# Optimization experiments

Measured on AMD Instinct MI355X. Metric: run time of the kernel, lower is better.

The kernel has to match this reference:

```python
import jax, jax.numpy as jnp
import numpy as np

WINDOW = 7
NUM_HEADS = 16
HEAD_DIM = 32  # dim 512 / 16 heads
SCALE = HEAD_DIM ** -0.5


def _relative_position_index(ws: int) -> np.ndarray:
    coords = np.stack(np.meshgrid(np.arange(ws), np.arange(ws), indexing='ij'))  # [2, ws, ws]
    flat = coords.reshape(2, -1)  # [2, N]
    rel = flat[:, :, None] - flat[:, None, :]  # [2, N, N]
    rel = rel.transpose(1, 2, 0)  # [N, N, 2]
    rh = (rel[:, :, 0] + ws - 1) * (2 * ws - 1)
    rw = rel[:, :, 1] + ws - 1
    return (rh + rw).astype(np.int32)  # [N, N]

REL_IDX = jnp.asarray(_relative_position_index(WINDOW))  # [49, 49]


def setup_inputs() -> dict:
    key = jax.random.key(0)
    ks = jax.random.split(key, 4)
    B, N, C = 4096, WINDOW * WINDOW, 512
    x = jax.random.normal(ks[0], (B, N, C), dtype=jnp.float32)
    qkv_w = jax.random.normal(ks[1], (C, 3 * C), dtype=jnp.float32) * (C ** -0.5)
    qkv_b = jnp.zeros((3 * C,), dtype=jnp.float32)
    proj_w = jax.random.normal(ks[2], (C, C), dtype=jnp.float32) * (C ** -0.5)
    proj_b = jnp.zeros((C,), dtype=jnp.float32)
    bias_table = jax.random.normal(ks[3], ((2 * WINDOW - 1) ** 2, NUM_HEADS), dtype=jnp.float32) * 0.02
    return {"x": x, "qkv_w": qkv_w, "qkv_b": qkv_b, "proj_w": proj_w,
            "proj_b": proj_b, "bias_table": bias_table}


def reference(x, qkv_w, qkv_b, proj_w, proj_b, bias_table):
    B, N, C = x.shape
    # QKV projection -> [B, N, 3, H, D] -> q/k/v [B, H, N, D]
    qkv = (x @ qkv_w + qkv_b).reshape(B, N, 3, NUM_HEADS, HEAD_DIM)
    qkv = jnp.transpose(qkv, (2, 0, 3, 1, 4))
    q, k, v = qkv[0], qkv[1], qkv[2]
    attn = jnp.einsum('bhnd,bhmd->bhnm', q * SCALE, k)  # [B, H, N, N]
    # relative position bias gather: [N*N, H] -> [1, H, N, N]
    bias = bias_table[REL_IDX.reshape(-1)].reshape(N, N, NUM_HEADS)
    attn = attn + jnp.transpose(bias, (2, 0, 1))[None]
    attn = jax.nn.softmax(attn, axis=-1)
    out = jnp.einsum('bhnm,bhmd->bhnd', attn, v)  # [B, H, N, D]
    out = jnp.transpose(out, (0, 2, 1, 3)).reshape(B, N, C)
    return out @ proj_w + proj_b
```

## Files before the change

kernel.cpp:

```cpp
#include <hip/hip_runtime.h>

typedef _Float16 h16;
typedef __attribute__((ext_vector_type(4))) _Float16 h16x4;
typedef __attribute__((ext_vector_type(8))) _Float16 h16x8;
typedef __attribute__((ext_vector_type(4))) float f32x4;

#define QSCALE 0.25505653882616254f
#define LOG2E  1.4426950408889634f
#define MFMA16(a, b, c) __builtin_amdgcn_mfma_f32_16x16x16f16(a, b, c, 0, 0, 0)
#define MFMA32(a, b, c) __builtin_amdgcn_mfma_f32_16x16x32_f16(a, b, c, 0, 0, 0)

#define O_BYTES 205520896ULL
#define W1F_OFF (O_BYTES)
#define W2T_OFF (W1F_OFF + 1572864ULL)
#define BF_OFF  (W2T_OFF + 524288ULL)

__global__ __launch_bounds__(256) void wa_prep(
    const float* __restrict__ qkv_w, const float* __restrict__ proj_w,
    const float* __restrict__ table,
    h16* __restrict__ w1F, h16* __restrict__ w2T, float* __restrict__ biasF) {
  __shared__ h16 T[32][33];
  const int b = blockIdx.x, tid = threadIdx.x;
  if (b < 256) {
    int tx = tid & 31, ty = tid >> 5;
    int bo = b & 15, bc = b >> 4;
    #pragma unroll
    for (int i = 0; i < 4; ++i) {
      int c = bc * 32 + ty + 8 * i, o = bo * 32 + tx;
      T[ty + 8 * i][tx] = (h16)proj_w[c * 512 + o];
    }
    __syncthreads();
    #pragma unroll
    for (int i = 0; i < 4; ++i) {
      int o_l = ty + 8 * i;
      w2T[(size_t)(bo * 32 + o_l) * 512 + bc * 32 + tx] = T[tx][o_l];
    }
  } else if (b < 640) {
    int chunk = (b - 256) * 256 + tid;
    int lane = chunk & 63;
    int rest = chunk >> 6;
    int f  = rest % 12;
    int kt = (rest / 12) & 7;
    int wv = (rest / 96) & 3;
    int g  = rest / 384;
    int s = f >> 2, d = (f >> 1) & 1, ks = f & 1;
    int l15 = lane & 15, lg = lane >> 4;
    int o = s * 512 + g * 128 + wv * 32 + d * 16 + l15;
    int k0 = kt * 64 + ks * 32 + lg * 8;
    float sc = (s == 0) ? QSCALE : 1.0f;
    h16x8 v;
    #pragma unroll
    for (int e = 0; e < 8; ++e)
      v[e] = (h16)(qkv_w[(size_t)(k0 + e) * 1536 + o] * sc);
    *(h16x8*)(w1F + (size_t)chunk * 8) = v;
  } else {
    int t = (b - 640) * 256 + tid;
    int lane = t & 63, jt = (t >> 6) & 3, qt = (t >> 8) & 3, head = t >> 10;
    int l15 = lane & 15, lg = lane >> 4;
    int q = qt * 16 + l15;
    float4 v;
    #pragma unroll
    for (int r = 0; r < 4; ++r) {
      int j = jt * 16 + lg * 4 + r;
      float val = -1e30f;
      if (j < 49 && q < 49) {
        int rel = (q / 7 - j / 7 + 6) * 13 + (q % 7 - j % 7 + 6);
        val = table[rel * 16 + head] * LOG2E;
      }
      ((float*)&v)[r] = val;
    }
    ((float4*)biasF)[t] = v;
  }
}

__global__ __launch_bounds__(256, 3) void wa_qkv_attn(
    const float* __restrict__ x, const float* __restrict__ qkv_b,
    const h16* __restrict__ w1F, const float* __restrict__ biasF,
    h16* __restrict__ O) {
  __shared__ __align__(16) char lds[50176];
  const int tid = threadIdx.x;
  const int wave = tid >> 6, lane = tid & 63;
  const int l15 = lane & 15, lg = lane >> 4;
  const int sw = l15 & 7;
  const int lbid = (blockIdx.x & 7) * 1024 + (blockIdx.x >> 3);
  const int w = lbid >> 1, gp = lbid & 1;
  const size_t rowbase = (size_t)w * 49;

  #pragma unroll
  for (int p = 0; p < 13; ++p) {
    int idx = tid + p * 256;
    if (idx < 3136) {
      int r = idx >> 6, c = idx & 63;
      const float* src = x + (rowbase + r) * 512 + c * 8;
      float4 a = *(const float4*)(src);
      float4 bb = *(const float4*)(src + 4);
      h16x8 h = { (h16)a.x, (h16)a.y, (h16)a.z, (h16)a.w,
                  (h16)bb.x, (h16)bb.y, (h16)bb.z, (h16)bb.w };
      *(h16x8*)(lds + r * 1024 + ((c ^ (r & 7)) << 4)) = h;
    }
  }
  __syncthreads();

  int xbA[4], xbB[4];
  #pragma unroll
  for (int t = 0; t < 4; ++t) {
    int row = (t < 3) ? (16 * t + l15) : 48;
    int swt = (t < 3) ? sw : 0;
    xbA[t] = row * 1024 + ((lg ^ swt) << 4);
    xbB[t] = row * 1024 + (((4 + lg) ^ swt) << 4);
  }
  const h16x4 ones = (h16x4){(h16)1.f, (h16)1.f, (h16)1.f, (h16)1.f};
  const float4* bF4 = (const float4*)biasF;

#define WLOAD8(DST, KT) {                                                  \
    _Pragma("unroll") for (int f8 = 0; f8 < 8; ++f8)                       \
      DST[f8] = *(const h16x8*)(wb + (size_t)(KT) * 6144 + f8 * 512); }

#define WLOAD4V(DST, KT) {                                                 \
    _Pragma("unroll") for (int f4 = 0; f4 < 4; ++f4)                       \
      DST[f4] = *(const h16x8*)(wb + (size_t)(KT) * 6144 + (8 + f4) * 512); }

#define STEP_QK(KT, W) {                                                   \
    h16x8 xf[4];                                                           \
    _Pragma("unroll") for (int t = 0; t < 4; ++t)                          \
      xf[t] = *(const h16x8*)(lds + xbA[t] + (KT) * 128);                  \
    __builtin_amdgcn_s_setprio(1);                                         \
    _Pragma("unroll") for (int d = 0; d < 2; ++d)                          \
    _Pragma("unroll") for (int t = 0; t < 4; ++t) {                        \
      accQ[d][t] = MFMA32(W[d*2],     xf[t], accQ[d][t]);                  \
      accK[d][t] = MFMA32(W[4 + d*2], xf[t], accK[d][t]);                  \
    }                                                                      \
    __builtin_amdgcn_s_setprio(0);                                         \
    _Pragma("unroll") for (int t = 0; t < 4; ++t)                          \
      xf[t] = *(const h16x8*)(lds + xbB[t] + (KT) * 128);                  \
    __builtin_amdgcn_s_setprio(1);                                         \
    _Pragma("unroll") for (int d = 0; d < 2; ++d)                          \
    _Pragma("unroll") for (int t = 0; t < 4; ++t) {                        \
      accQ[d][t] = MFMA32(W[d*2 + 1],     xf[t], accQ[d][t]);              \
      accK[d][t] = MFMA32(W[4 + d*2 + 1], xf[t], accK[d][t]);              \
    }                                                                      \
    __builtin_amdgcn_s_setprio(0); }

#define STEP_V(KT, W) {                                                    \
    h16x8 xf[4];                                                           \
    _Pragma("unroll") for (int t = 0; t < 4; ++t)                          \
      xf[t] = *(const h16x8*)(lds + xbA[t] + (KT) * 128);                  \
    __builtin_amdgcn_s_setprio(1);                                         \
    _Pragma("unroll") for (int d = 0; d < 2; ++d)                          \
    _Pragma("unroll") for (int t = 0; t < 4; ++t)                          \
      accV[t][d] = MFMA32(xf[t], W[d*2], accV[t][d]);                      \
    __builtin_amdgcn_s_setprio(0);                                         \
    _Pragma("unroll") for (int t = 0; t < 4; ++t)                          \
      xf[t] = *(const h16x8*)(lds + xbB[t] + (KT) * 128);                  \
    __builtin_amdgcn_s_setprio(1);                                         \
    _Pragma("unroll") for (int d = 0; d < 2; ++d)                          \
    _Pragma("unroll") for (int t = 0; t < 4; ++t)                          \
      accV[t][d] = MFMA32(xf[t], W[d*2 + 1], accV[t][d]);                  \
    __builtin_amdgcn_s_setprio(0); }

#define PROCESS_HEAD(G) {                                                  \
    const int head = (G) * 4 + wave;                                       \
    const h16* wb = w1F + ((size_t)((G) * 4 + wave) * 8) * 6144 + lane * 8;\
    h16x4 Qh[2][4], Kh[2][4], Vh[4][2];                                    \
     {                          \
      f32x4 accQ[2][4], accK[2][4];                                        \
      _Pragma("unroll") for (int d = 0; d < 2; ++d)                        \
      _Pragma("unroll") for (int t = 0; t < 4; ++t) {                      \
        accQ[d][t] = (f32x4){0.f, 0.f, 0.f, 0.f};                          \
        accK[d][t] = (f32x4){0.f, 0.f, 0.f, 0.f};                          \
      }                                                                    \
      h16x8 WA[8], WB[8];                                                  \
      WLOAD8(WA, 0);                                                       \
      for (int kt2 = 0; kt2 < 4; ++kt2) {                                  \
        WLOAD8(WB, 2 * kt2 + 1);                                           \
        STEP_QK(2 * kt2, WA);                                              \
        if (kt2 < 3) WLOAD8(WA, 2 * kt2 + 2);                              \
        STEP_QK(2 * kt2 + 1, WB);                                          \
      }                                                                    \
      _Pragma("unroll") for (int d = 0; d < 2; ++d) {                      \
        float bq[4], bk[4];                                                \
        _Pragma("unroll") for (int r = 0; r < 4; ++r) {                    \
          bq[r] = qkv_b[head * 32 + 16 * d + 4 * lg + r] * QSCALE;         \
          bk[r] = qkv_b[512 + head * 32 + 16 * d + 4 * lg + r];            \
        }                                                                  \
        _Pragma("unroll") for (int t = 0; t < 4; ++t)                      \
        _Pragma("unroll") for (int r = 0; r < 4; ++r) {                    \
          Qh[d][t][r] = (h16)(accQ[d][t][r] + bq[r]);                      \
          Kh[d][t][r] = (h16)(accK[d][t][r] + bk[r]);                      \
        }                                                                  \
      }                                                                    \
    }                                                                      \
     {                  \
      f32x4 accV[4][2];                                                    \
      _Pragma("unroll") for (int t = 0; t < 4; ++t)                        \
      _Pragma("unroll") for (int d = 0; d < 2; ++d)                        \
        accV[t][d] = (f32x4){0.f, 0.f, 0.f, 0.f};                          \
      h16x8 VA[4], VB[4];                                                  \
      WLOAD4V(VA, 0);                                                      \
      for (int kt2 = 0; kt2 < 4; ++kt2) {                                  \
        WLOAD4V(VB, 2 * kt2 + 1);                                          \
        STEP_V(2 * kt2, VA);                                               \
        if (kt2 < 3) WLOAD4V(VA, 2 * kt2 + 2);                             \
        STEP_V(2 * kt2 + 1, VB);                                           \
      }                                                                    \
      _Pragma("unroll") for (int d = 0; d < 2; ++d) {                      \
        float bv = qkv_b[1024 + head * 32 + 16 * d + l15];                 \
        _Pragma("unroll") for (int t = 0; t < 4; ++t)                      \
        _Pragma("unroll") for (int r = 0; r < 4; ++r)                      \
          Vh[t][d][r] = (h16)(accV[t][d][r] + bv);                         \
      }                                                                    \
    }                                                                      \
                             \
    f32x4 st[4][4];                                                        \
    __builtin_amdgcn_s_setprio(1);                                         \
    _Pragma("unroll") for (int jt = 0; jt < 4; ++jt)                       \
    _Pragma("unroll") for (int qt = 0; qt < 4; ++qt) {                     \
      float4 bvv = bF4[(head * 16 + qt * 4 + jt) * 64 + lane];             \
      f32x4 c0 = { bvv.x, bvv.y, bvv.z, bvv.w };                           \
      st[jt][qt] = MFMA16(Kh[0][jt], Qh[0][qt], c0);                       \
      st[jt][qt] = MFMA16(Kh[1][jt], Qh[1][qt], st[jt][qt]);               \
    }                                                                      \
    __builtin_amdgcn_s_setprio(0);                                         \
    h16x4 pf[4][4];                                                        \
    _Pragma("unroll") for (int qt = 0; qt < 4; ++qt)                       \
    _Pragma("unroll") for (int jt = 0; jt < 4; ++jt) {                     \
      h16x4 p;                                                             \
      _Pragma("unroll") for (int r = 0; r < 4; ++r)                        \
        p[r] = (h16)exp2f(st[jt][qt][r]);                                  \
      pf[jt][qt] = p;                                                      \
    }                                                                      \
    f32x4 ss[4];                                                           \
    _Pragma("unroll") for (int qt = 0; qt < 4; ++qt)                       \
      ss[qt] = (f32x4){0.f, 0.f, 0.f, 0.f};                                \
    f32x4 ot[2][4];                                                        \
    _Pragma("unroll") for (int d = 0; d < 2; ++d)                          \
    _Pragma("unroll") for (int qt = 0; qt < 4; ++qt)                       \
      ot[d][qt] = (f32x4){0.f, 0.f, 0.f, 0.f};                             \
    __builtin_amdgcn_s_setprio(1);                                         \
    _Pragma("unroll") for (int jt = 0; jt < 4; ++jt)                       \
    _Pragma("unroll") for (int qt = 0; qt < 4; ++qt) {                     \
      ss[qt] = MFMA16(ones, pf[jt][qt], ss[qt]);                           \
      _Pragma("unroll") for (int d = 0; d < 2; ++d)                        \
        ot[d][qt] = MFMA16(Vh[jt][d], pf[jt][qt], ot[d][qt]);              \
    }                                                                      \
    __builtin_amdgcn_s_setprio(0);                                         \
    _Pragma("unroll") for (int qt = 0; qt < 4; ++qt) {                     \
      int q = 16 * qt + l15;                                               \
      float ri = 1.0f / ss[qt][0];                                         \
      if (q < 49) {                                                        \
        h16* gdst = O + (rowbase + q) * 512 + head * 32 + 4 * lg;          \
        _Pragma("unroll") for (int d = 0; d < 2; ++d) {                    \
          h16x4 ov;                                                        \
          _Pragma("unroll") for (int r = 0; r < 4; ++r)                    \
            ov[r] = (h16)(ot[d][qt][r] * ri);                              \
          *(h16x4*)(gdst + 16 * d) = ov;                                   \
        }                                                                  \
      }                                                                    \
    } }

  PROCESS_HEAD(gp * 2);
  PROCESS_HEAD(gp * 2 + 1);
#undef PROCESS_HEAD
#undef STEP_QK
#undef STEP_V
#undef WLOAD8
#undef WLOAD4V
}

__global__ __launch_bounds__(256, 3) void wa_proj(
    const h16* __restrict__ O, const h16* __restrict__ w2T,
    const float* __restrict__ proj_b, float* __restrict__ out) {
  __shared__ __align__(16) char lds[32768];
  char* Ac = lds;
  char* Bc = lds + 16384;
  const int tid = threadIdx.x;
  const int wave = tid >> 6, lane = tid & 63;
  const int l15 = lane & 15, lg = lane >> 4;
  const int lbid = (blockIdx.x & 7) * 784 + (blockIdx.x >> 3);
  const int rowt = lbid >> 2, colt = lbid & 3;
  const int wr = wave >> 1, wc = wave & 1;

  f32x4 acc[4][4];
  #pragma unroll
  for (int a = 0; a < 4; ++a)
    #pragma unroll
    for (int b = 0; b < 4; ++b) acc[a][b] = (f32x4){0.f, 0.f, 0.f, 0.f};

  h16x8 pre[8];
  #pragma unroll
  for (int p = 0; p < 8; ++p) {
    int idx = tid + p * 256;
    int r = (idx >> 3) & 127, c = idx & 7;
    pre[p] = (idx < 1024)
        ? *(const h16x8*)(O   + (size_t)(rowt * 128 + r) * 512 + c * 8)
        : *(const h16x8*)(w2T + (size_t)(colt * 128 + r) * 512 + c * 8);
  }
  #pragma unroll
  for (int p = 0; p < 8; ++p) {
    int idx = tid + p * 256;
    int r = (idx >> 3) & 127, c = idx & 7;
    char* dst = ((idx < 1024) ? Ac : Bc) + r * 128 + ((c ^ (r & 7)) << 4);
    *(h16x8*)dst = pre[p];
  }
  __syncthreads();

  for (int kt = 0; kt < 8; ++kt) {
    if (kt < 7) {
      #pragma unroll
      for (int p = 0; p < 8; ++p) {
        int idx = tid + p * 256;
        int r = (idx >> 3) & 127, c = idx & 7;
        pre[p] = (idx < 1024)
            ? *(const h16x8*)(O   + (size_t)(rowt * 128 + r) * 512 + (kt + 1) * 64 + c * 8)
            : *(const h16x8*)(w2T + (size_t)(colt * 128 + r) * 512 + (kt + 1) * 64 + c * 8);
      }
    }
    #pragma unroll
    for (int kh = 0; kh < 2; ++kh) {
      const int cc = kh * 4 + lg;
      const int sw = (l15 & 7);
      h16x8 af[4], bf[4];
      #pragma unroll
      for (int mt = 0; mt < 4; ++mt) {
        int r = wr * 64 + 16 * mt + l15;
        af[mt] = *(const h16x8*)(Ac + r * 128 + ((cc ^ sw) << 4));
      }
      #pragma unroll
      for (int nt = 0; nt < 4; ++nt) {
        int r = wc * 64 + 16 * nt + l15;
        bf[nt] = *(const h16x8*)(Bc + r * 128 + ((cc ^ sw) << 4));
      }
      __builtin_amdgcn_s_setprio(1);
      #pragma unroll
      for (int mt = 0; mt < 4; ++mt)
        #pragma unroll
        for (int nt = 0; nt < 4; ++nt)
          acc[mt][nt] = MFMA32(af[mt], bf[nt], acc[mt][nt]);
      __builtin_amdgcn_s_setprio(0);
    }
    __syncthreads();
    if (kt < 7) {
      #pragma unroll
      for (int p = 0; p < 8; ++p) {
        int idx = tid + p * 256;
        int r = (idx >> 3) & 127, c = idx & 7;
        char* dst = ((idx < 1024) ? Ac : Bc) + r * 128 + ((c ^ (r & 7)) << 4);
        *(h16x8*)dst = pre[p];
      }
      __syncthreads();
    }
  }
  #pragma unroll
  for (int nt = 0; nt < 4; ++nt) {
    int col = colt * 128 + wc * 64 + nt * 16 + l15;
    float pb = proj_b[col];
    #pragma unroll
    for (int mt = 0; mt < 4; ++mt) {
      int row = rowt * 128 + wr * 64 + mt * 16 + 4 * lg;
      #pragma unroll
      for (int r = 0; r < 4; ++r)
        out[(size_t)(row + r) * 512 + col] = acc[mt][nt][r] + pb;
    }
  }
}

extern "C" void kernel_launch(void* const* d_in, const int* in_sizes, int n_in,
                              void* d_out, int out_size, void* d_ws, size_t ws_size,
                              hipStream_t stream) {
  const float* x          = (const float*)d_in[0];
  const float* qkv_w      = (const float*)d_in[1];
  const float* qkv_b      = (const float*)d_in[2];
  const float* proj_w     = (const float*)d_in[3];
  const float* proj_b     = (const float*)d_in[4];
  const float* bias_table = (const float*)d_in[5];
  float* out = (float*)d_out;

  char* ws = (char*)d_ws;
  h16*   O     = (h16*)ws;
  h16*   w1F   = (h16*)(ws + W1F_OFF);
  h16*   w2T   = (h16*)(ws + W2T_OFF);
  float* biasF = (float*)(ws + BF_OFF);

  wa_prep<<<704, 256, 0, stream>>>(qkv_w, proj_w, bias_table, w1F, w2T, biasF);
  wa_qkv_attn<<<8192, 256, 0, stream>>>(x, qkv_b, w1F, biasF, O);
  wa_proj<<<1568 * 4, 256, 0, stream>>>(O, w2T, proj_b, out);
}
```

Baseline: 701.1 us.

## Pre-swizzle proj weights into MFMA fragment layout and drop double-buffered QKV loads

The prep kernel now writes proj_w directly in MFMA B-fragment order, so the projection kernel reads B operands straight from global memory (L2) instead of staging them through LDS. This halves the projection kernel's LDS footprint and its staging traffic, at the cost of uncoalesced-per-iteration global fragment loads that are not prefetched. Separately, the QKV/attention kernel replaces its software double-buffered weight loads with a simple non-unrolled loop that loads and consumes one k-tile at a time. That lowers register pressure but exposes the weight-load latency.

After: 699.3 us. About the same (-0.3%).

```diff
diff --git a/kernel.cpp b/kernel.cpp
--- a/kernel.cpp
+++ b/kernel.cpp
@@ -12,31 +12,30 @@
 
 #define O_BYTES 205520896ULL
 #define W1F_OFF (O_BYTES)
-#define W2T_OFF (W1F_OFF + 1572864ULL)
-#define BF_OFF  (W2T_OFF + 524288ULL)
+#define W2F_OFF (W1F_OFF + 1572864ULL)
+#define BF_OFF  (W2F_OFF + 524288ULL)
 
 __global__ __launch_bounds__(256) void wa_prep(
     const float* __restrict__ qkv_w, const float* __restrict__ proj_w,
     const float* __restrict__ table,
-    h16* __restrict__ w1F, h16* __restrict__ w2T, float* __restrict__ biasF) {
-  __shared__ h16 T[32][33];
+    h16* __restrict__ w1F, h16* __restrict__ w2F, float* __restrict__ biasF) {
   const int b = blockIdx.x, tid = threadIdx.x;
-  if (b < 256) {
-    int tx = tid & 31, ty = tid >> 5;
-    int bo = b & 15, bc = b >> 4;
-    #pragma unroll
-    for (int i = 0; i < 4; ++i) {
-      int c = bc * 32 + ty + 8 * i, o = bo * 32 + tx;
-      T[ty + 8 * i][tx] = (h16)proj_w[c * 512 + o];
-    }
-    __syncthreads();
-    #pragma unroll
-    for (int i = 0; i < 4; ++i) {
-      int o_l = ty + 8 * i;
-      w2T[(size_t)(bo * 32 + o_l) * 512 + bc * 32 + tx] = T[tx][o_l];
-    }
-  } else if (b < 640) {
-    int chunk = (b - 256) * 256 + tid;
+  if (b < 128) {
+    int chunk = b * 256 + tid;
+    int lane = chunk & 63;
+    int rest = chunk >> 6;
+    int fr = rest & 7, kt = (rest >> 3) & 7, cw = rest >> 6;
+    int nt = fr >> 1, kh = fr & 1;
+    int l15 = lane & 15, lg = lane >> 4;
+    int o = cw * 64 + nt * 16 + l15;
+    int k0 = kt * 64 + (kh * 4 + lg) * 8;
+    h16x8 v;
+    #pragma unroll
+    for (int e = 0; e < 8; ++e)
+      v[e] = (h16)proj_w[(size_t)(k0 + e) * 512 + o];
+    *(h16x8*)(w2F + (size_t)chunk * 8) = v;
+  } else if (b < 512) {
+    int chunk = (b - 128) * 256 + tid;
     int lane = chunk & 63;
     int rest = chunk >> 6;
     int f  = rest % 12;
@@ -54,7 +53,7 @@
       v[e] = (h16)(qkv_w[(size_t)(k0 + e) * 1536 + o] * sc);
     *(h16x8*)(w1F + (size_t)chunk * 8) = v;
   } else {
-    int t = (b - 640) * 256 + tid;
+    int t = (b - 512) * 256 + tid;
     int lane = t & 63, jt = (t >> 6) & 3, qt = (t >> 8) & 3, head = t >> 10;
     int l15 = lane & 15, lg = lane >> 4;
     int q = qt * 16 + l15;
@@ -162,20 +161,17 @@
     const int head = (G) * 4 + wave;                                       \
     const h16* wb = w1F + ((size_t)((G) * 4 + wave) * 8) * 6144 + lane * 8;\
     h16x4 Qh[2][4], Kh[2][4], Vh[4][2];                                    \
-     {                          \
+     {       \
       f32x4 accQ[2][4], accK[2][4];                                        \
       _Pragma("unroll") for (int d = 0; d < 2; ++d)                        \
       _Pragma("unroll") for (int t = 0; t < 4; ++t) {                      \
         accQ[d][t] = (f32x4){0.f, 0.f, 0.f, 0.f};                          \
         accK[d][t] = (f32x4){0.f, 0.f, 0.f, 0.f};                          \
       }                                                                    \
-      h16x8 WA[8], WB[8];                                                  \
-      WLOAD8(WA, 0);                                                       \
-      for (int kt2 = 0; kt2 < 4; ++kt2) {                                  \
-        WLOAD8(WB, 2 * kt2 + 1);                                           \
-        STEP_QK(2 * kt2, WA);                                              \
-        if (kt2 < 3) WLOAD8(WA, 2 * kt2 + 2);                              \
-        STEP_QK(2 * kt2 + 1, WB);                                          \
+      _Pragma("unroll 1") for (int kt = 0; kt < 8; ++kt) {                 \
+        h16x8 WQK[8];                                                      \
+        WLOAD8(WQK, kt);                                                   \
+        STEP_QK(kt, WQK);                                                  \
       }                                                                    \
       _Pragma("unroll") for (int d = 0; d < 2; ++d) {                      \
         float bq[4], bk[4];                                                \
@@ -190,18 +186,15 @@
         }                                                                  \
       }                                                                    \
     }                                                                      \
-     {                  \
+     { \
       f32x4 accV[4][2];                                                    \
       _Pragma("unroll") for (int t = 0; t < 4; ++t)                        \
       _Pragma("unroll") for (int d = 0; d < 2; ++d)                        \
         accV[t][d] = (f32x4){0.f, 0.f, 0.f, 0.f};                          \
-      h16x8 VA[4], VB[4];                                                  \
-      WLOAD4V(VA, 0);                                                      \
-      for (int kt2 = 0; kt2 < 4; ++kt2) {                                  \
-        WLOAD4V(VB, 2 * kt2 + 1);                                          \
-        STEP_V(2 * kt2, VA);                                               \
-        if (kt2 < 3) WLOAD4V(VA, 2 * kt2 + 2);                             \
-        STEP_V(2 * kt2 + 1, VB);                                           \
+      _Pragma("unroll 1") for (int kt = 0; kt < 8; ++kt) {                 \
+        h16x8 WV[4];                                                       \
+        WLOAD4V(WV, kt);                                                   \
+        STEP_V(kt, WV);                                                    \
       }                                                                    \
       _Pragma("unroll") for (int d = 0; d < 2; ++d) {                      \
         float bv = qkv_b[1024 + head * 32 + 16 * d + l15];                 \
@@ -268,17 +261,16 @@
 }
 
 __global__ __launch_bounds__(256, 3) void wa_proj(
-    const h16* __restrict__ O, const h16* __restrict__ w2T,
+    const h16* __restrict__ O, const h16* __restrict__ w2F,
     const float* __restrict__ proj_b, float* __restrict__ out) {
-  __shared__ __align__(16) char lds[32768];
-  char* Ac = lds;
-  char* Bc = lds + 16384;
+  __shared__ __align__(16) char lds[16384];
   const int tid = threadIdx.x;
   const int wave = tid >> 6, lane = tid & 63;
   const int l15 = lane & 15, lg = lane >> 4;
   const int lbid = (blockIdx.x & 7) * 784 + (blockIdx.x >> 3);
   const int rowt = lbid >> 2, colt = lbid & 3;
   const int wr = wave >> 1, wc = wave & 1;
+  const h16* wb2 = w2F + (size_t)(colt * 2 + wc) * 32768 + lane * 8;
 
   f32x4 acc[4][4];
   #pragma unroll
@@ -286,50 +278,42 @@
     #pragma unroll
     for (int b = 0; b < 4; ++b) acc[a][b] = (f32x4){0.f, 0.f, 0.f, 0.f};
 
-  h16x8 pre[8];
-  #pragma unroll
-  for (int p = 0; p < 8; ++p) {
+  h16x8 pre[4];
+  #pragma unroll
+  for (int p = 0; p < 4; ++p) {
     int idx = tid + p * 256;
-    int r = (idx >> 3) & 127, c = idx & 7;
-    pre[p] = (idx < 1024)
-        ? *(const h16x8*)(O   + (size_t)(rowt * 128 + r) * 512 + c * 8)
-        : *(const h16x8*)(w2T + (size_t)(colt * 128 + r) * 512 + c * 8);
-  }
-  #pragma unroll
-  for (int p = 0; p < 8; ++p) {
+    int r = idx >> 3, c = idx & 7;
+    pre[p] = *(const h16x8*)(O + (size_t)(rowt * 128 + r) * 512 + c * 8);
+  }
+  #pragma unroll
+  for (int p = 0; p < 4; ++p) {
     int idx = tid + p * 256;
-    int r = (idx >> 3) & 127, c = idx & 7;
-    char* dst = ((idx < 1024) ? Ac : Bc) + r * 128 + ((c ^ (r & 7)) << 4);
-    *(h16x8*)dst = pre[p];
+    int r = idx >> 3, c = idx & 7;
+    *(h16x8*)(lds + r * 128 + ((c ^ (r & 7)) << 4)) = pre[p];
   }
   __syncthreads();
 
   for (int kt = 0; kt < 8; ++kt) {
     if (kt < 7) {
       #pragma unroll
-      for (int p = 0; p < 8; ++p) {
+      for (int p = 0; p < 4; ++p) {
         int idx = tid + p * 256;
-        int r = (idx >> 3) & 127, c = idx & 7;
-        pre[p] = (idx < 1024)
-            ? *(const h16x8*)(O   + (size_t)(rowt * 128 + r) * 512 + (kt + 1) * 64 + c * 8)
-            : *(const h16x8*)(w2T + (size_t)(colt * 128 + r) * 512 + (kt + 1) * 64 + c * 8);
+        int r = idx >> 3, c = idx & 7;
+        pre[p] = *(const h16x8*)(O + (size_t)(rowt * 128 + r) * 512 + (kt + 1) * 64 + c * 8);
       }
     }
     #pragma unroll
     for (int kh = 0; kh < 2; ++kh) {
-      const int cc = kh * 4 + lg;
       const int sw = (l15 & 7);
       h16x8 af[4], bf[4];
       #pragma unroll
       for (int mt = 0; mt < 4; ++mt) {
         int r = wr * 64 + 16 * mt + l15;
-        af[mt] = *(const h16x8*)(Ac + r * 128 + ((cc ^ sw) << 4));
+        af[mt] = *(const h16x8*)(lds + r * 128 + (((kh * 4 + lg) ^ sw) << 4));
       }
       #pragma unroll
-      for (int nt = 0; nt < 4; ++nt) {
-        int r = wc * 64 + 16 * nt + l15;
-        bf[nt] = *(const h16x8*)(Bc + r * 128 + ((cc ^ sw) << 4));
-      }
+      for (int nt = 0; nt < 4; ++nt)
+        bf[nt] = *(const h16x8*)(wb2 + (size_t)(kt * 8 + nt * 2 + kh) * 512);
       __builtin_amdgcn_s_setprio(1);
       #pragma unroll
       for (int mt = 0; mt < 4; ++mt)
@@ -341,11 +325,10 @@
     __syncthreads();
     if (kt < 7) {
       #pragma unroll
-      for (int p = 0; p < 8; ++p) {
+      for (int p = 0; p < 4; ++p) {
         int idx = tid + p * 256;
-        int r = (idx >> 3) & 127, c = idx & 7;
-        char* dst = ((idx < 1024) ? Ac : Bc) + r * 128 + ((c ^ (r & 7)) << 4);
-        *(h16x8*)dst = pre[p];
+        int r = idx >> 3, c = idx & 7;
+        *(h16x8*)(lds + r * 128 + ((c ^ (r & 7)) << 4)) = pre[p];
       }
       __syncthreads();
     }
@@ -378,10 +361,10 @@
   char* ws = (char*)d_ws;
   h16*   O     = (h16*)ws;
   h16*   w1F   = (h16*)(ws + W1F_OFF);
-  h16*   w2T   = (h16*)(ws + W2T_OFF);
+  h16*   w2F   = (h16*)(ws + W2F_OFF);
   float* biasF = (float*)(ws + BF_OFF);
 
-  wa_prep<<<704, 256, 0, stream>>>(qkv_w, proj_w, bias_table, w1F, w2T, biasF);
+  wa_prep<<<576, 256, 0, stream>>>(qkv_w, proj_w, bias_table, w1F, w2F, biasF);
   wa_qkv_attn<<<8192, 256, 0, stream>>>(x, qkv_b, w1F, biasF, O);
-  wa_proj<<<1568 * 4, 256, 0, stream>>>(O, w2T, proj_b, out);
+  wa_proj<<<1568 * 4, 256, 0, stream>>>(O, w2F, proj_b, out);
 }
```
